# Kernel optimization log

Hardware: AMD Instinct MI355X
Metric: run time of the kernel (lower is better)

Reference implementation:

```python
import jax, jax.numpy as jnp
import numpy as np

ALPHA = 0.99  # EMA decay used in ewa_func


def setup_inputs() -> dict:
    key = jax.random.key(0)
    k1, k2 = jax.random.split(key)
    N, K, D = 65536, 2048, 128  # flattened latents, vq_num, vq_dim
    initrange = 1.0 / D  # matches init_embed uniform_(-1/vq_dim, 1/vq_dim)
    return {
        "Z": jax.random.normal(k1, (N, D), dtype=jnp.float32),
        "dict_val": jax.random.uniform(k2, (K, D), dtype=jnp.float32,
                                       minval=-initrange, maxval=initrange),
        "dict_cnt": jnp.ones((K,), dtype=jnp.float32),
    }


def reference(Z, dict_val, dict_cnt):
    K, D = dict_val.shape
    # pairwise squared L2 dist: ((Z[:,None]-W[None,:])**2).sum(2), computed as
    # ||z||^2 - 2 z.w + ||w||^2 (same math, GEMM-efficient form)
    z2 = jnp.sum(Z * Z, axis=1)                      # [N]
    w2 = jnp.sum(dict_val * dict_val, axis=1)        # [K]
    dist = z2[:, None] - 2.0 * (Z @ dict_val.T) + w2[None, :]  # [N, K]
    i = jnp.argmin(dist, axis=1)                     # [N] assigned codes

    # EMA codebook update, only for clusters that received assignments
    counts = jax.ops.segment_sum(jnp.ones((Z.shape[0],), Z.dtype), i, num_segments=K)  # [K]
    sums = jax.ops.segment_sum(Z, i, num_segments=K)  # [K, D]
    assigned = counts > 0
    c_new = jnp.where(assigned, ALPHA * dict_cnt + (1.0 - ALPHA) * counts, dict_cnt)
    w_new = jnp.where(
        assigned[:, None],
        ALPHA * dict_val + (1.0 - ALPHA) * sums / jnp.maximum(c_new, 1e-12)[:, None],
        dict_val,
    )

    W_j = w_new[i]                                   # [N, D] quantized vectors
    # straight-through estimator: forward = W_j (detached), grad passes to Z
    st_out = Z + jax.lax.stop_gradient(W_j - Z)
    # commit_loss = L2_dist(Z, sg(W_j)).sum(1).mean()
    diff = Z - jax.lax.stop_gradient(W_j)
    commit_loss = jnp.mean(jnp.sum(diff * diff, axis=1))
    return st_out, commit_loss, w_new, c_new
```

## Files before the change

### kernel.cpp

```cpp
#include <hip/hip_runtime.h>
#include <hip/hip_bf16.h>

#define NN 65536
#define KK 2048
#define DD 128

typedef __attribute__((ext_vector_type(8))) _Float16 f16x8;
typedef __attribute__((ext_vector_type(16))) float f32x16;

static __device__ __forceinline__ unsigned encf(float f) {
    unsigned u = __float_as_uint(f);
    return u ^ (((unsigned)((int)u >> 31)) | 0x80000000u);
}

static __device__ __forceinline__ void gll16(const void* g, void* l) {
    __builtin_amdgcn_global_load_lds(
        (const __attribute__((address_space(1))) void*)g,
        (__attribute__((address_space(3))) void*)l, 16, 0, 0);
}

__global__ __launch_bounds__(256) void vq_prep(const float* __restrict__ Z,
                                               const float* __restrict__ Wd,
                                               _Float16* __restrict__ Zre,
                                               _Float16* __restrict__ Wre,
                                               float* __restrict__ w2,
                                               float* __restrict__ bins)
{
    int tid = threadIdx.x;
    int rl = tid >> 4, c = tid & 15;
    int row = blockIdx.x * 16 + rl;
    bool isW = row >= NN;
    int r = isW ? row - NN : row;
    const float* src = isW ? Wd : Z;

    const float4* zp = reinterpret_cast<const float4*>(src + (size_t)r * DD + c * 8);
    float4 v0 = zp[0], v1 = zp[1];
    float v[8] = {v0.x, v0.y, v0.z, v0.w, v1.x, v1.y, v1.z, v1.w};

    float scale = isW ? 128.0f : 1.0f;
    f16x8 hv;
#pragma unroll
    for (int j = 0; j < 8; ++j) hv[j] = (_Float16)(v[j] * scale);

    float p = 0.f;
#pragma unroll
    for (int j = 0; j < 8; ++j) p = fmaf(v[j], v[j], p);
#pragma unroll
    for (int off2 = 1; off2 < 16; off2 <<= 1) p += __shfl_xor(p, off2, 64);

    int t = c >> 1, g = c & 1;
    if (!isW) {
        size_t off = (size_t)(r >> 5) * 4096 + t * 512 + g * 256 + (size_t)(r & 31) * 8;
        *reinterpret_cast<f16x8*>(Zre + off) = hv;
        __shared__ float sb[16];
        if (c == 0) sb[rl] = p;
        __syncthreads();
        if (tid == 0) {
            float s = 0.f;
#pragma unroll
            for (int i = 0; i < 16; ++i) s += sb[i];
            atomicAdd(&bins[(blockIdx.x & 63) * 16], s);
        }
    } else {
        size_t off = (size_t)(r >> 7) * 16384 + (size_t)((r >> 5) & 3) * 4096
                   + t * 512 + g * 256 + (size_t)(r & 31) * 8;
        *reinterpret_cast<f16x8*>(Wre + off) = hv;
        if (c == 0) w2[r] = p;
    }
}

__global__ __launch_bounds__(256, 2) void vq_gemm(const _Float16* __restrict__ Zre,
                                                  const _Float16* __restrict__ Wre,
                                                  const float* __restrict__ w2,
                                                  const float* __restrict__ Z,
                                                  const float* __restrict__ Wd,
                                                  int* __restrict__ assign,
                                                  float* __restrict__ counts)
{
    int rb  = blockIdx.x;
    int tid = threadIdx.x;
    int wid = tid >> 6, lane = tid & 63;
    int g2 = lane >> 5, l31 = lane & 31;

    __shared__ _Float16 Bs[2][16384];
    __shared__ float W2s[2048];
    __shared__ float2 T2s[128];

    const _Float16* zb = Zre + ((size_t)rb * 4 + wid) * 4096;
    f16x8 a[8];
#pragma unroll
    for (int t = 0; t < 8; ++t)
        a[t] = *reinterpret_cast<const f16x8*>(zb + t * 512 + g2 * 256 + l31 * 8);

    const float INF = __uint_as_float(0x7F800000u);
    float t1[16], t2[16];
#pragma unroll
    for (int s = 0; s < 16; ++s) { t1[s] = INF; t2[s] = INF; }

    const f32x16 zz = {};

#pragma unroll
    for (int j = 0; j < 2; ++j)
        gll16(w2 + j * 1024 + tid * 4, &W2s[j * 1024 + tid * 4]);
#pragma unroll
    for (int j = 0; j < 8; ++j)
        gll16(Wre + j * 2048 + tid * 8, &Bs[0][j * 2048 + tid * 8]);

#define EPI(ACC, W2V, CI)                                                      \
    _Pragma("unroll")                                                          \
    for (int r = 0; r < 16; ++r) {                                             \
        float d = fmaf(-0.015625f, (ACC)[r], (W2V));                           \
        float df = __uint_as_float((__float_as_uint(d) & 0xFFFFF800u) | (CI)); \
        t2[r] = __builtin_amdgcn_fmed3f(df, t1[r], t2[r]);                     \
        t1[r] = fminf(t1[r], df);                                              \
    }

#define STEP(IT, CUR)                                                          \
    do {                                                                       \
        if ((IT) < 15) {                                                       \
            const _Float16* wb = Wre + (size_t)((IT) + 1) * 16384;             \
            _Float16* ld = Bs[(CUR) ^ 1];                                      \
            _Pragma("unroll")                                                  \
            for (int j = 0; j < 8; ++j)                                        \
                gll16(wb + j * 2048 + tid * 8, ld + j * 2048 + tid * 8);       \
            asm volatile("s_waitcnt vmcnt(8)" ::: "memory");                   \
        } else {                                                               \
            asm volatile("s_waitcnt vmcnt(0)" ::: "memory");                   \
        }                                                                      \
        __builtin_amdgcn_s_barrier();                                          \
        {                                                                      \
            const _Float16* bb = &Bs[(CUR)][g2 * 256 + l31 * 8];               \
            float w2v0 = W2s[(IT) * 128 + l31];                                \
            float w2v1 = W2s[(IT) * 128 + 32 + l31];                           \
            float w2v2 = W2s[(IT) * 128 + 64 + l31];                           \
            float w2v3 = W2s[(IT) * 128 + 96 + l31];                           \
            f16x8 bE[8], bO[8];                                                \
            f32x16 acc0, acc1, acc2, acc3;                                     \
            _Pragma("unroll")                                                  \
            for (int t = 0; t < 8; ++t) {                                      \
                bE[t] = *reinterpret_cast<const f16x8*>(bb + t * 512);         \
                bO[t] = *reinterpret_cast<const f16x8*>(bb + 4096 + t * 512);  \
            }                                                                  \
            _Pragma("unroll")                                                  \
            for (int t = 0; t < 8; ++t)                                        \
                acc0 = __builtin_amdgcn_mfma_f32_32x32x16_f16(                 \
                    a[t], bE[t], (t == 0) ? zz : acc0, 0, 0, 0);               \
            _Pragma("unroll")                                                  \
            for (int t = 0; t < 8; ++t)                                        \
                bE[t] = *reinterpret_cast<const f16x8*>(bb + 8192 + t * 512);  \
            _Pragma("unroll")                                                  \
            for (int t = 0; t < 8; ++t)                                        \
                acc1 = __builtin_amdgcn_mfma_f32_32x32x16_f16(                 \
                    a[t], bO[t], (t == 0) ? zz : acc1, 0, 0, 0);               \
            unsigned cib = (unsigned)((IT) * 128) + (unsigned)l31;             \
            EPI(acc0, w2v0, cib)                                               \
            _Pragma("unroll")                                                  \
            for (int t = 0; t < 8; ++t)                                        \
                bO[t] = *reinterpret_cast<const f16x8*>(bb + 12288 + t * 512); \
            _Pragma("unroll")                                                  \
            for (int t = 0; t < 8; ++t)                                        \
                acc2 = __builtin_amdgcn_mfma_f32_32x32x16_f16(                 \
                    a[t], bE[t], (t == 0) ? zz : acc2, 0, 0, 0);               \
            EPI(acc1, w2v1, cib + 32)                                          \
            _Pragma("unroll")                                                  \
            for (int t = 0; t < 8; ++t)                                        \
                acc3 = __builtin_amdgcn_mfma_f32_32x32x16_f16(                 \
                    a[t], bO[t], (t == 0) ? zz : acc3, 0, 0, 0);               \
            EPI(acc2, w2v2, cib + 64)                                          \
            EPI(acc3, w2v3, cib + 96)                                          \
        }                                                                      \
        __builtin_amdgcn_s_barrier();                                          \
    } while (0)

#pragma unroll 1
    for (int ip = 0; ip < 8; ++ip) {
        STEP(2 * ip, 0);
        STEP(2 * ip + 1, 1);
    }
#undef STEP
#undef EPI

#pragma unroll
    for (int s = 0; s < 16; ++s) {
        float v1 = t1[s], v2 = t2[s];
#pragma unroll
        for (int msk = 1; msk < 32; msk <<= 1) {
            float o1 = __shfl_xor(v1, msk, 64);
            float o2 = __shfl_xor(v2, msk, 64);
            float mx = fmaxf(v1, o1);
            v1 = fminf(v1, o1);
            v2 = fminf(fminf(v2, o2), mx);
        }
        if (l31 == 0) {
            int rl = wid * 32 + (s & 3) + 8 * (s >> 2) + 4 * g2;
            T2s[rl] = make_float2(v1, v2);
        }
    }
    __syncthreads();

    if (tid < 128) {
        int row = rb * 128 + tid;
        float2 t2v = T2s[tid];
        unsigned u1 = __float_as_uint(t2v.x);
        unsigned u2 = __float_as_uint(t2v.y);
        int c1 = (int)(u1 & 2047u), c2 = (int)(u2 & 2047u);
        float d1 = __uint_as_float(u1 & 0xFFFFF800u);
        float d2 = __uint_as_float(u2 & 0xFFFFF800u);

        int res = c1;
        if (d2 - d1 <= 1e-3f) {
            int cols[2] = {c1, c2};
            const float4* zp = reinterpret_cast<const float4*>(Z + (size_t)row * DD);
            float s0 = 0.f, s1 = 0.f, s2 = 0.f, s3 = 0.f;
            for (int q = 0; q < 32; ++q) {
                float4 z = zp[q];
                s0 = fmaf(z.x, z.x, s0);
                s1 = fmaf(z.y, z.y, s1);
                s2 = fmaf(z.z, z.z, s2);
                s3 = fmaf(z.w, z.w, s3);
            }
            float z2v = (s0 + s1) + (s2 + s3);
            unsigned long long be = ~0ull;
            for (int i = 0; i < 2; ++i) {
                int k = cols[i];
                const float4* wp = reinterpret_cast<const float4*>(Wd + (size_t)k * DD);
                float a0 = 0.f, a1 = 0.f, a2 = 0.f, a3 = 0.f;
                for (int q = 0; q < 32; ++q) {
                    float4 zq = zp[q];
                    float4 wq = wp[q];
                    a0 = fmaf(zq.x, wq.x, a0);
                    a1 = fmaf(zq.y, wq.y, a1);
                    a2 = fmaf(zq.z, wq.z, a2);
                    a3 = fmaf(zq.w, wq.w, a3);
                }
                float sdot = (a0 + a1) + (a2 + a3);
                float tt = __fsub_rn(z2v, __fmul_rn(2.0f, sdot));
                float dist = __fadd_rn(tt, W2s[k]);
                unsigned long long key =
                    (((unsigned long long)encf(dist)) << 32) | (unsigned)k;
                if (key < be) be = key;
            }
            res = (int)(be & 0xffffffffu);
        }
        assign[row] = res;
        atomicAdd(&counts[res], 1.0f);
    }
}

__global__ __launch_bounds__(256) void vq_scan(const float* __restrict__ counts,
                                               int* __restrict__ start,
                                               int* __restrict__ cursor)
{
    __shared__ int ps[256];
    int tid = threadIdx.x;
    int c[8];
    int tot = 0;
#pragma unroll
    for (int j = 0; j < 8; ++j) { c[j] = (int)counts[tid * 8 + j]; tot += c[j]; }
    ps[tid] = tot;
    __syncthreads();
    for (int off = 1; off < 256; off <<= 1) {
        int v = (tid >= off) ? ps[tid - off] : 0;
        __syncthreads();
        ps[tid] += v;
        __syncthreads();
    }
    int base = ps[tid] - tot;
#pragma unroll
    for (int j = 0; j < 8; ++j) {
        start[tid * 8 + j] = base;
        cursor[tid * 8 + j] = base;
        base += c[j];
    }
}

__global__ __launch_bounds__(256) void vq_permute(const int* __restrict__ assign,
                                                  int* __restrict__ cursor,
                                                  int* __restrict__ order)
{
    int row = blockIdx.x * 256 + threadIdx.x;
    int k = assign[row];
    int pos = atomicAdd(&cursor[k], 1);
    order[pos] = row;
}

__global__ __launch_bounds__(128) void vq_accum_update(const float* __restrict__ Z,
                                                       const float* __restrict__ Wd,
                                                       const float* __restrict__ dict_cnt,
                                                       const float* __restrict__ counts,
                                                       const int* __restrict__ start,
                                                       const int* __restrict__ order,
                                                       float* __restrict__ w_new_out,
                                                       float* __restrict__ c_new_out,
                                                       float* __restrict__ st_out,
                                                       float* __restrict__ bins)
{
    int k = blockIdx.x;
    int d = threadIdx.x;
    int n = (int)counts[k];
    int st = start[k];

    float sum = 0.f;
    int i = 0;
    for (; i + 4 <= n; i += 4) {
        int o0 = order[st + i + 0];
        int o1 = order[st + i + 1];
        int o2 = order[st + i + 2];
        int o3 = order[st + i + 3];
        float v0 = Z[(size_t)o0 * DD + d];
        float v1 = Z[(size_t)o1 * DD + d];
        float v2 = Z[(size_t)o2 * DD + d];
        float v3 = Z[(size_t)o3 * DD + d];
        sum += (v0 + v1) + (v2 + v3);
    }
    for (; i < n; ++i)
        sum += Z[(size_t)order[st + i] * DD + d];

    float cnt = dict_cnt[k];
    float ck = counts[k];
    bool assigned = n > 0;
    float cn = assigned ? __fadd_rn(__fmul_rn(0.99f, cnt), __fmul_rn(0.01f, ck)) : cnt;
    float w = Wd[(size_t)k * DD + d];
    float wn = w;
    if (assigned) {
        float num = __fmul_rn(0.01f, sum);
        wn = __fadd_rn(__fmul_rn(0.99f, w), num / fmaxf(cn, 1e-12f));
    }
    w_new_out[(size_t)k * DD + d] = wn;
    if (d == 0) c_new_out[k] = cn;

    int j = 0;
    for (; j + 4 <= n; j += 4) {
        int o0 = order[st + j + 0];
        int o1 = order[st + j + 1];
        int o2 = order[st + j + 2];
        int o3 = order[st + j + 3];
        st_out[(size_t)o0 * DD + d] = wn;
        st_out[(size_t)o1 * DD + d] = wn;
        st_out[(size_t)o2 * DD + d] = wn;
        st_out[(size_t)o3 * DD + d] = wn;
    }
    for (; j < n; ++j)
        st_out[(size_t)order[st + j] * DD + d] = wn;

    float p = wn * fmaf(ck, wn, -2.0f * sum);
#pragma unroll
    for (int off = 32; off; off >>= 1) p += __shfl_down(p, off, 64);
    __shared__ float sm[2];
    if ((threadIdx.x & 63) == 0) sm[threadIdx.x >> 6] = p;
    __syncthreads();
    if (threadIdx.x == 0) atomicAdd(&bins[(64 + (k & 63)) * 16], sm[0] + sm[1]);
}

__global__ void vq_finish(const float* __restrict__ bins,
                          float* __restrict__ out_loss)
{
    if (threadIdx.x == 0) {
        float s = 0.f;
        for (int i = 0; i < 128; ++i) s += bins[i * 16];
        out_loss[0] = s * (1.0f / 65536.0f);
    }
}

extern "C" void kernel_launch(void* const* d_in, const int* in_sizes, int n_in,
                              void* d_out, int out_size, void* d_ws, size_t ws_size,
                              hipStream_t stream)
{
    const float* Z        = (const float*)d_in[0];
    const float* Wd       = (const float*)d_in[1];
    const float* dict_cnt = (const float*)d_in[2];

    float* out      = (float*)d_out;
    float* st_out   = out;
    float* out_loss = out + (size_t)NN * DD;
    float* w_new    = out_loss + 1;
    float* c_new    = w_new + (size_t)KK * DD;

    char* ws = (char*)d_ws;
    _Float16* Zre  = (_Float16*)ws;
    _Float16* Wre  = (_Float16*)(ws + 16777216);
    float* w2      = (float*)(ws + 17301504);
    int* assign    = (int*)(ws + 17309696);
    float* counts  = (float*)(ws + 17571840);
    float* bins    = (float*)(ws + 17580032);
    int* start     = (int*)(ws + 17588224);
    int* cursor    = (int*)(ws + 17596416);
    int* order     = (int*)(ws + 17604608);

    hipMemsetAsync(counts, 0, 8192 + 8192, stream);

    vq_prep<<<(NN + KK) / 16, 256, 0, stream>>>(Z, Wd, Zre, Wre, w2, bins);
    vq_gemm<<<NN / 128, 256, 0, stream>>>(Zre, Wre, w2, Z, Wd, assign, counts);
    vq_scan<<<1, 256, 0, stream>>>(counts, start, cursor);
    vq_permute<<<NN / 256, 256, 0, stream>>>(assign, cursor, order);
    vq_accum_update<<<KK, 128, 0, stream>>>(Z, Wd, dict_cnt, counts, start, order,
                                            w_new, c_new, st_out, bins);
    vq_finish<<<1, 64, 0, stream>>>(bins, out_loss);
}
```

Before: 114.3 us.

## Drop Z fp16 pre-pass, load Z directly in GEMM, read codebook from global

```diff
diff --git a/kernel.cpp b/kernel.cpp
--- a/kernel.cpp
+++ b/kernel.cpp
@@ -19,28 +19,20 @@
         (__attribute__((address_space(3))) void*)l, 16, 0, 0);
 }
 
-__global__ __launch_bounds__(256) void vq_prep(const float* __restrict__ Z,
-                                               const float* __restrict__ Wd,
-                                               _Float16* __restrict__ Zre,
+__global__ __launch_bounds__(256) void vq_prep(const float* __restrict__ Wd,
                                                _Float16* __restrict__ Wre,
-                                               float* __restrict__ w2,
-                                               float* __restrict__ bins)
+                                               float* __restrict__ w2)
 {
     int tid = threadIdx.x;
     int rl = tid >> 4, c = tid & 15;
-    int row = blockIdx.x * 16 + rl;
-    bool isW = row >= NN;
-    int r = isW ? row - NN : row;
-    const float* src = isW ? Wd : Z;
-
-    const float4* zp = reinterpret_cast<const float4*>(src + (size_t)r * DD + c * 8);
-    float4 v0 = zp[0], v1 = zp[1];
+    int r = blockIdx.x * 16 + rl;
+    const float4* wp = reinterpret_cast<const float4*>(Wd + (size_t)r * DD + c * 8);
+    float4 v0 = wp[0], v1 = wp[1];
     float v[8] = {v0.x, v0.y, v0.z, v0.w, v1.x, v1.y, v1.z, v1.w};
 
-    float scale = isW ? 128.0f : 1.0f;
     f16x8 hv;
 #pragma unroll
-    for (int j = 0; j < 8; ++j) hv[j] = (_Float16)(v[j] * scale);
+    for (int j = 0; j < 8; ++j) hv[j] = (_Float16)(v[j] * 128.0f);
 
     float p = 0.f;
 #pragma unroll
@@ -49,48 +41,45 @@
     for (int off2 = 1; off2 < 16; off2 <<= 1) p += __shfl_xor(p, off2, 64);
 
     int t = c >> 1, g = c & 1;
-    if (!isW) {
-        size_t off = (size_t)(r >> 5) * 4096 + t * 512 + g * 256 + (size_t)(r & 31) * 8;
-        *reinterpret_cast<f16x8*>(Zre + off) = hv;
-        __shared__ float sb[16];
-        if (c == 0) sb[rl] = p;
-        __syncthreads();
-        if (tid == 0) {
-            float s = 0.f;
-#pragma unroll
-            for (int i = 0; i < 16; ++i) s += sb[i];
-            atomicAdd(&bins[(blockIdx.x & 63) * 16], s);
-        }
-    } else {
-        size_t off = (size_t)(r >> 7) * 16384 + (size_t)((r >> 5) & 3) * 4096
-                   + t * 512 + g * 256 + (size_t)(r & 31) * 8;
-        *reinterpret_cast<f16x8*>(Wre + off) = hv;
-        if (c == 0) w2[r] = p;
-    }
-}
-
-__global__ __launch_bounds__(256, 2) void vq_gemm(const _Float16* __restrict__ Zre,
-                                                  const _Float16* __restrict__ Wre,
-                                                  const float* __restrict__ w2,
-                                                  const float* __restrict__ Z,
-                                                  const float* __restrict__ Wd,
-                                                  int* __restrict__ assign,
-                                                  float* __restrict__ counts)
+    size_t off = (size_t)(r >> 7) * 16384 + (size_t)((r >> 5) & 3) * 4096
+               + t * 512 + g * 256 + (size_t)(r & 31) * 8;
+    *reinterpret_cast<f16x8*>(Wre + off) = hv;
+    if (c == 0) w2[r] = p;
+}
+
+__global__ __launch_bounds__(256) void vq_gemm(const float* __restrict__ Z,
+                                               const _Float16* __restrict__ Wre,
+                                               const float* __restrict__ w2g,
+                                               const float* __restrict__ Wd,
+                                               int* __restrict__ assign,
+                                               float* __restrict__ counts)
 {
     int rb  = blockIdx.x;
     int tid = threadIdx.x;
     int wid = tid >> 6, lane = tid & 63;
+    int rg = wid >> 1, wc = wid & 1;
     int g2 = lane >> 5, l31 = lane & 31;
 
-    __shared__ _Float16 Bs[2][16384];
     __shared__ float W2s[2048];
-    __shared__ float2 T2s[128];
-
-    const _Float16* zb = Zre + ((size_t)rb * 4 + wid) * 4096;
+    __shared__ float2 T2s[2][64];
+
+#pragma unroll
+    for (int j = 0; j < 2; ++j)
+        gll16(w2g + j * 1024 + tid * 4, &W2s[j * 1024 + tid * 4]);
+
+    const float* zrow = Z + ((size_t)(rb * 64 + rg * 32 + l31)) * DD + g2 * 8;
     f16x8 a[8];
 #pragma unroll
-    for (int t = 0; t < 8; ++t)
-        a[t] = *reinterpret_cast<const f16x8*>(zb + t * 512 + g2 * 256 + l31 * 8);
+    for (int t = 0; t < 8; ++t) {
+        float4 u0 = *reinterpret_cast<const float4*>(zrow + t * 16);
+        float4 u1 = *reinterpret_cast<const float4*>(zrow + t * 16 + 4);
+        f16x8 h;
+        h[0] = (_Float16)u0.x; h[1] = (_Float16)u0.y;
+        h[2] = (_Float16)u0.z; h[3] = (_Float16)u0.w;
+        h[4] = (_Float16)u1.x; h[5] = (_Float16)u1.y;
+        h[6] = (_Float16)u1.z; h[7] = (_Float16)u1.w;
+        a[t] = h;
+    }
 
     const float INF = __uint_as_float(0x7F800000u);
     float t1[16], t2[16];
@@ -99,12 +88,8 @@
 
     const f32x16 zz = {};
 
-#pragma unroll
-    for (int j = 0; j < 2; ++j)
-        gll16(w2 + j * 1024 + tid * 4, &W2s[j * 1024 + tid * 4]);
-#pragma unroll
-    for (int j = 0; j < 8; ++j)
-        gll16(Wre + j * 2048 + tid * 8, &Bs[0][j * 2048 + tid * 8]);
+    asm volatile("s_waitcnt vmcnt(0)" ::: "memory");
+    __builtin_amdgcn_s_barrier();
 
 #define EPI(ACC, W2V, CI)                                                      \
     _Pragma("unroll")                                                          \
@@ -115,69 +100,48 @@
         t1[r] = fminf(t1[r], df);                                              \
     }
 
-#define STEP(IT, CUR)                                                          \
-    do {                                                                       \
-        if ((IT) < 15) {                                                       \
-            const _Float16* wb = Wre + (size_t)((IT) + 1) * 16384;             \
-            _Float16* ld = Bs[(CUR) ^ 1];                                      \
-            _Pragma("unroll")                                                  \
-            for (int j = 0; j < 8; ++j)                                        \
-                gll16(wb + j * 2048 + tid * 8, ld + j * 2048 + tid * 8);       \
-            asm volatile("s_waitcnt vmcnt(8)" ::: "memory");                   \
-        } else {                                                               \
-            asm volatile("s_waitcnt vmcnt(0)" ::: "memory");                   \
-        }                                                                      \
-        __builtin_amdgcn_s_barrier();                                          \
-        {                                                                      \
-            const _Float16* bb = &Bs[(CUR)][g2 * 256 + l31 * 8];               \
-            float w2v0 = W2s[(IT) * 128 + l31];                                \
-            float w2v1 = W2s[(IT) * 128 + 32 + l31];                           \
-            float w2v2 = W2s[(IT) * 128 + 64 + l31];                           \
-            float w2v3 = W2s[(IT) * 128 + 96 + l31];                           \
-            f16x8 bE[8], bO[8];                                                \
-            f32x16 acc0, acc1, acc2, acc3;                                     \
-            _Pragma("unroll")                                                  \
-            for (int t = 0; t < 8; ++t) {                                      \
-                bE[t] = *reinterpret_cast<const f16x8*>(bb + t * 512);         \
-                bO[t] = *reinterpret_cast<const f16x8*>(bb + 4096 + t * 512);  \
-            }                                                                  \
-            _Pragma("unroll")                                                  \
-            for (int t = 0; t < 8; ++t)                                        \
-                acc0 = __builtin_amdgcn_mfma_f32_32x32x16_f16(                 \
-                    a[t], bE[t], (t == 0) ? zz : acc0, 0, 0, 0);               \
-            _Pragma("unroll")                                                  \
-            for (int t = 0; t < 8; ++t)                                        \
-                bE[t] = *reinterpret_cast<const f16x8*>(bb + 8192 + t * 512);  \
-            _Pragma("unroll")                                                  \
-            for (int t = 0; t < 8; ++t)                                        \
-                acc1 = __builtin_amdgcn_mfma_f32_32x32x16_f16(                 \
-                    a[t], bO[t], (t == 0) ? zz : acc1, 0, 0, 0);               \
-            unsigned cib = (unsigned)((IT) * 128) + (unsigned)l31;             \
-            EPI(acc0, w2v0, cib)                                               \
-            _Pragma("unroll")                                                  \
-            for (int t = 0; t < 8; ++t)                                        \
-                bO[t] = *reinterpret_cast<const f16x8*>(bb + 12288 + t * 512); \
-            _Pragma("unroll")                                                  \
-            for (int t = 0; t < 8; ++t)                                        \
-                acc2 = __builtin_amdgcn_mfma_f32_32x32x16_f16(                 \
-                    a[t], bE[t], (t == 0) ? zz : acc2, 0, 0, 0);               \
-            EPI(acc1, w2v1, cib + 32)                                          \
-            _Pragma("unroll")                                                  \
-            for (int t = 0; t < 8; ++t)                                        \
-                acc3 = __builtin_amdgcn_mfma_f32_32x32x16_f16(                 \
-                    a[t], bO[t], (t == 0) ? zz : acc3, 0, 0, 0);               \
-            EPI(acc2, w2v2, cib + 64)                                          \
-            EPI(acc3, w2v3, cib + 96)                                          \
-        }                                                                      \
-        __builtin_amdgcn_s_barrier();                                          \
-    } while (0)
-
+    const _Float16* bbase = Wre + g2 * 256 + l31 * 8;
 #pragma unroll 1
-    for (int ip = 0; ip < 8; ++ip) {
-        STEP(2 * ip, 0);
-        STEP(2 * ip + 1, 1);
-    }
-#undef STEP
+    for (int i = 0; i < 8; ++i) {
+        int cb = wc * 8 + i;
+        const _Float16* bp = bbase + (size_t)cb * 16384;
+        unsigned cib = (unsigned)(cb * 128) + (unsigned)l31;
+        float w2v0 = W2s[cb * 128 + l31];
+        float w2v1 = W2s[cb * 128 + 32 + l31];
+        float w2v2 = W2s[cb * 128 + 64 + l31];
+        float w2v3 = W2s[cb * 128 + 96 + l31];
+
+        f16x8 b[8];
+        f32x16 acc;
+#pragma unroll
+        for (int t = 0; t < 8; ++t)
+            b[t] = *reinterpret_cast<const f16x8*>(bp + t * 512);
+#pragma unroll
+        for (int t = 0; t < 8; ++t)
+            acc = __builtin_amdgcn_mfma_f32_32x32x16_f16(a[t], b[t], (t == 0) ? zz : acc, 0, 0, 0);
+        EPI(acc, w2v0, cib)
+#pragma unroll
+        for (int t = 0; t < 8; ++t)
+            b[t] = *reinterpret_cast<const f16x8*>(bp + 4096 + t * 512);
+#pragma unroll
+        for (int t = 0; t < 8; ++t)
+            acc = __builtin_amdgcn_mfma_f32_32x32x16_f16(a[t], b[t], (t == 0) ? zz : acc, 0, 0, 0);
+        EPI(acc, w2v1, cib + 32)
+#pragma unroll
+        for (int t = 0; t < 8; ++t)
+            b[t] = *reinterpret_cast<const f16x8*>(bp + 8192 + t * 512);
+#pragma unroll
+        for (int t = 0; t < 8; ++t)
+            acc = __builtin_amdgcn_mfma_f32_32x32x16_f16(a[t], b[t], (t == 0) ? zz : acc, 0, 0, 0);
+        EPI(acc, w2v2, cib + 64)
+#pragma unroll
+        for (int t = 0; t < 8; ++t)
+            b[t] = *reinterpret_cast<const f16x8*>(bp + 12288 + t * 512);
+#pragma unroll
+        for (int t = 0; t < 8; ++t)
+            acc = __builtin_amdgcn_mfma_f32_32x32x16_f16(a[t], b[t], (t == 0) ? zz : acc, 0, 0, 0);
+        EPI(acc, w2v3, cib + 96)
+    }
 #undef EPI
 
 #pragma unroll
@@ -192,17 +156,21 @@
             v2 = fminf(fminf(v2, o2), mx);
         }
         if (l31 == 0) {
-            int rl = wid * 32 + (s & 3) + 8 * (s >> 2) + 4 * g2;
-            T2s[rl] = make_float2(v1, v2);
+            int rl = rg * 32 + (s & 3) + 8 * (s >> 2) + 4 * g2;
+            T2s[wc][rl] = make_float2(v1, v2);
         }
     }
     __syncthreads();
 
-    if (tid < 128) {
-        int row = rb * 128 + tid;
-        float2 t2v = T2s[tid];
-        unsigned u1 = __float_as_uint(t2v.x);
-        unsigned u2 = __float_as_uint(t2v.y);
+    if (tid < 64) {
+        int row = rb * 64 + tid;
+        float2 pa = T2s[0][tid];
+        float2 pb = T2s[1][tid];
+        float v1 = fminf(pa.x, pb.x);
+        float v2 = fminf(fmaxf(pa.x, pb.x), fminf(pa.y, pb.y));
+
+        unsigned u1 = __float_as_uint(v1);
+        unsigned u2 = __float_as_uint(v2);
         int c1 = (int)(u1 & 2047u), c2 = (int)(u2 & 2047u);
         float d1 = __uint_as_float(u1 & 0xFFFFF800u);
         float d2 = __uint_as_float(u2 & 0xFFFFF800u);
@@ -300,7 +268,7 @@
     int n = (int)counts[k];
     int st = start[k];
 
-    float sum = 0.f;
+    float sum = 0.f, sq = 0.f;
     int i = 0;
     for (; i + 4 <= n; i += 4) {
         int o0 = order[st + i + 0];
@@ -312,9 +280,16 @@
         float v2 = Z[(size_t)o2 * DD + d];
         float v3 = Z[(size_t)o3 * DD + d];
         sum += (v0 + v1) + (v2 + v3);
-    }
-    for (; i < n; ++i)
-        sum += Z[(size_t)order[st + i] * DD + d];
+        sq = fmaf(v0, v0, sq);
+        sq = fmaf(v1, v1, sq);
+        sq = fmaf(v2, v2, sq);
+        sq = fmaf(v3, v3, sq);
+    }
+    for (; i < n; ++i) {
+        float v = Z[(size_t)order[st + i] * DD + d];
+        sum += v;
+        sq = fmaf(v, v, sq);
+    }
 
     float cnt = dict_cnt[k];
     float ck = counts[k];
@@ -343,13 +318,13 @@
     for (; j < n; ++j)
         st_out[(size_t)order[st + j] * DD + d] = wn;
 
-    float p = wn * fmaf(ck, wn, -2.0f * sum);
+    float p = fmaf(ck, wn * wn, fmaf(-2.0f * wn, sum, sq));
 #pragma unroll
     for (int off = 32; off; off >>= 1) p += __shfl_down(p, off, 64);
     __shared__ float sm[2];
     if ((threadIdx.x & 63) == 0) sm[threadIdx.x >> 6] = p;
     __syncthreads();
-    if (threadIdx.x == 0) atomicAdd(&bins[(64 + (k & 63)) * 16], sm[0] + sm[1]);
+    if (threadIdx.x == 0) atomicAdd(&bins[(k & 63) * 16], sm[0] + sm[1]);
 }
 
 __global__ void vq_finish(const float* __restrict__ bins,
@@ -357,7 +332,7 @@
 {
     if (threadIdx.x == 0) {
         float s = 0.f;
-        for (int i = 0; i < 128; ++i) s += bins[i * 16];
+        for (int i = 0; i < 64; ++i) s += bins[i * 16];
         out_loss[0] = s * (1.0f / 65536.0f);
     }
 }
@@ -377,20 +352,19 @@
     float* c_new    = w_new + (size_t)KK * DD;
 
     char* ws = (char*)d_ws;
-    _Float16* Zre  = (_Float16*)ws;
-    _Float16* Wre  = (_Float16*)(ws + 16777216);
-    float* w2      = (float*)(ws + 17301504);
-    int* assign    = (int*)(ws + 17309696);
-    float* counts  = (float*)(ws + 17571840);
-    float* bins    = (float*)(ws + 17580032);
-    int* start     = (int*)(ws + 17588224);
-    int* cursor    = (int*)(ws + 17596416);
-    int* order     = (int*)(ws + 17604608);
-
-    hipMemsetAsync(counts, 0, 8192 + 8192, stream);
-
-    vq_prep<<<(NN + KK) / 16, 256, 0, stream>>>(Z, Wd, Zre, Wre, w2, bins);
-    vq_gemm<<<NN / 128, 256, 0, stream>>>(Zre, Wre, w2, Z, Wd, assign, counts);
+    _Float16* Wre  = (_Float16*)ws;
+    float* w2      = (float*)(ws + 524288);
+    int* assign    = (int*)(ws + 532480);
+    float* counts  = (float*)(ws + 794624);
+    float* bins    = (float*)(ws + 802816);
+    int* start     = (int*)(ws + 806912);
+    int* cursor    = (int*)(ws + 815104);
+    int* order     = (int*)(ws + 823296);
+
+    hipMemsetAsync(counts, 0, 8192 + 4096, stream);
+
+    vq_prep<<<KK / 16, 256, 0, stream>>>(Wd, Wre, w2);
+    vq_gemm<<<NN / 64, 256, 0, stream>>>(Z, Wre, w2, Wd, assign, counts);
     vq_scan<<<1, 256, 0, stream>>>(counts, start, cursor);
     vq_permute<<<NN / 256, 256, 0, stream>>>(assign, cursor, order);
     vq_accum_update<<<KK, 128, 0, stream>>>(Z, Wd, dict_cnt, counts, start, order,
```

New measurement: 189.0 us. 1.65x slower.
